# Performance work log

Measured on AMD Instinct MI355X. Metric: run time of the kernel, lower is better.

## Reference

```python
import jax, jax.numpy as jnp
import numpy as np

ALPHA = 0.2          # LeakyReLU negative slope
NEG = -9e15          # masking value from the torch source


def _gat_multihead(x, adj, W, a):
    """All nheads GATLayers (concat=True math, elu applied by caller).
    x: [B,N,F], adj: [B,N,N], W: [H,F,O], a: [H,2O]. Returns [B,H,N,O].
    Note a_input @ a decomposes as h_i.a[:O] + h_j.a[O:], so we never
    materialize the O(N^2 * 2O) pairwise concat tensor."""
    h = jnp.einsum('bnf,hfo->bhno', x, W)            # [B,H,N,O]
    O = h.shape[-1]
    s1 = jnp.einsum('bhno,ho->bhn', h, a[:, :O])     # h_i . a_src
    s2 = jnp.einsum('bhno,ho->bhn', h, a[:, O:])     # h_j . a_dst
    e = jax.nn.leaky_relu(s1[..., :, None] + s2[..., None, :], ALPHA)  # [B,H,N,N]
    att = jax.nn.softmax(jnp.where(adj[:, None] > 0, e, NEG), axis=-1)
    return jnp.einsum('bhij,bhjo->bhio', att, h)


def _gat_single(x, adj, W, a):
    """out_att GATLayer (concat=False, no elu). W: [F,O], a: [2O]."""
    h = jnp.einsum('bnf,fo->bno', x, W)
    O = W.shape[-1]
    s1 = h @ a[:O]
    s2 = h @ a[O:]
    e = jax.nn.leaky_relu(s1[:, :, None] + s2[:, None, :], ALPHA)
    att = jax.nn.softmax(jnp.where(adj > 0, e, NEG), axis=-1)
    return jnp.einsum('bij,bjo->bio', att, h)


def setup_inputs() -> dict:
    key = jax.random.key(0)
    ks = jax.random.split(key, 10)
    B, N, F = 2, 2048, 768
    H, O = 8, 256
    x = jax.random.normal(ks[0], (B, N, F), dtype=jnp.float32)
    # sparse-ish binary adjacency (adj>0 is all that matters) + self loops
    adj = (jax.random.uniform(ks[1], (B, N, N)) < 0.05).astype(jnp.float32)
    adj = jnp.maximum(adj, jnp.eye(N, dtype=jnp.float32)[None])
    mask = jnp.ones((B, N, 1), dtype=jnp.float32)  # unused by GAT.forward
    s = 0.05
    W_heads = jax.random.normal(ks[2], (H, F, O), dtype=jnp.float32) * s
    a_heads = jax.random.normal(ks[3], (H, 2 * O), dtype=jnp.float32) * s
    W_out = jax.random.normal(ks[4], (H * O, O), dtype=jnp.float32) * s
    a_out = jax.random.normal(ks[5], (2 * O,), dtype=jnp.float32) * s
    W_lin = jax.random.normal(ks[6], (O, H * O), dtype=jnp.float32) * s  # nn.Linear weight [out,in]
    b_lin = jnp.zeros((O,), dtype=jnp.float32)
    W_ln = jax.random.normal(ks[7], (O, O), dtype=jnp.float32) * s
    b_ln = jnp.zeros((O,), dtype=jnp.float32)
    return {"x": x, "adj": adj, "mask": mask, "W_heads": W_heads,
            "a_heads": a_heads, "W_out": W_out, "a_out": a_out,
            "W_lin": W_lin, "b_lin": b_lin, "W_ln": W_ln, "b_ln": b_ln}


def reference(x, adj, mask, W_heads, a_heads, W_out, a_out, W_lin, b_lin, W_ln, b_ln):
    # layer 0: multi-head GAT, elu, concat over heads (dropout=0 in eval)
    hp = jax.nn.elu(_gat_multihead(x, adj, W_heads, a_heads))  # [B,H,N,O]
    B, H, N, O = hp.shape
    x1 = jnp.transpose(hp, (0, 2, 1, 3)).reshape(B, N, H * O)
    # layer 1: residual linear + out_att (concat=False)
    x2 = x1 @ W_lin.T + b_lin + _gat_single(x1, adj, W_out, a_out)
    # final: relu(ln(x))
    return jax.nn.relu(x2 @ W_ln.T + b_ln)
```

## Files before the change

### kernel.cpp

```cpp
#include <hip/hip_runtime.h>
#include <hip/hip_bf16.h>

constexpr int Bb = 2, Nn = 2048, Ff = 768, Hh = 8, Oo = 256;

typedef __attribute__((ext_vector_type(8)))  short   short8;
typedef __attribute__((ext_vector_type(16))) float   f32x16;
typedef __attribute__((ext_vector_type(4)))  unsigned short ushort4_t;

__device__ inline unsigned short f2bf(float f) {
    unsigned u = __float_as_uint(f);
    u = (u + 0x7FFFu + ((u >> 16) & 1u)) >> 16;
    return (unsigned short)u;
}

__global__ __launch_bounds__(256) void adjbits_kernel(
        const float* __restrict__ adj, unsigned long long* __restrict__ bits) {
    size_t gid = (size_t)blockIdx.x * 256 + threadIdx.x;
    float v = adj[gid];
    unsigned long long m = __ballot(v > 0.f);
    if ((threadIdx.x & 63) == 0) bits[gid >> 6] = m;
}

__global__ __launch_bounds__(256) void cast_bf_kernel(
        const float* __restrict__ in, unsigned short* __restrict__ out) {
    size_t i = (size_t)blockIdx.x * 256 + threadIdx.x;
    float4 v = ((const float4*)in)[i];
    ushort4_t o;
    o.x = f2bf(v.x); o.y = f2bf(v.y); o.z = f2bf(v.z); o.w = f2bf(v.w);
    ((ushort4_t*)out)[i] = o;
}

__global__ __launch_bounds__(256) void wfrag_kn_kernel(
        const float* __restrict__ W, unsigned short* __restrict__ out,
        int K, int N, long long sW, long long sO) {
    W   += (size_t)blockIdx.y * sW;
    out += (size_t)blockIdx.y * sO;
    int t = threadIdx.x;
    int f = blockIdx.x * 4 + (t >> 6);
    int slot = t & 63, kh = slot >> 5, lm = slot & 31;
    int nfk = K >> 4;
    int nt = f / nfk, kt = f - nt * nfk;
    const float* wp = W + (size_t)(kt * 16 + kh * 8) * N + nt * 32 + lm;
    ushort4_t o0, o1;
    o0.x = f2bf(wp[0]);             o0.y = f2bf(wp[(size_t)N]);
    o0.z = f2bf(wp[2 * (size_t)N]); o0.w = f2bf(wp[3 * (size_t)N]);
    o1.x = f2bf(wp[4 * (size_t)N]); o1.y = f2bf(wp[5 * (size_t)N]);
    o1.z = f2bf(wp[6 * (size_t)N]); o1.w = f2bf(wp[7 * (size_t)N]);
    unsigned short* op = out + (size_t)f * 512 + slot * 8;
    *(ushort4_t*)op = o0;
    *(ushort4_t*)(op + 4) = o1;
}

__global__ __launch_bounds__(256) void wfrag_nk_kernel(
        const float* __restrict__ W, unsigned short* __restrict__ out, int K) {
    int t = threadIdx.x;
    int f = blockIdx.x * 4 + (t >> 6);
    int slot = t & 63, kh = slot >> 5, lm = slot & 31;
    int nfk = K >> 4;
    int nt = f / nfk, kt = f - nt * nfk;
    const float* wp = W + (size_t)(nt * 32 + lm) * K + kt * 16 + kh * 8;
    float4 a = *(const float4*)wp, b = *(const float4*)(wp + 4);
    ushort4_t o0, o1;
    o0.x = f2bf(a.x); o0.y = f2bf(a.y); o0.z = f2bf(a.z); o0.w = f2bf(a.w);
    o1.x = f2bf(b.x); o1.y = f2bf(b.y); o1.z = f2bf(b.z); o1.w = f2bf(b.w);
    unsigned short* op = out + (size_t)f * 512 + slot * 8;
    *(ushort4_t*)op = o0;
    *(ushort4_t*)(op + 4) = o1;
}

__global__ __launch_bounds__(256) void gemm_bf_kernel(
        const unsigned short* __restrict__ A, int K, long long sA, int bAshift,
        const unsigned short* __restrict__ BF, long long sB, int bmask,
        float* __restrict__ C, long long sC,
        unsigned short* __restrict__ CF, long long sCF, int Mtot,
        const float* __restrict__ bias, int mode,
        const float* __restrict__ aall, int amask,
        float* __restrict__ E1p, float* __restrict__ E1n, float2* __restrict__ E2pn) {
    int z = blockIdx.z;
    A  += (size_t)(z >> bAshift) * sA;
    BF += (size_t)(z & bmask) * sB;
    if (C) C += (size_t)z * sC;
    if (CF) CF += (size_t)z * sCF;
    int m0 = blockIdx.x * 64;
    int t = threadIdx.x;
    int wv = t >> 6, lane = t & 63;
    int lm = lane & 31, kh = lane >> 5;
    int nfk = K >> 4;
    __shared__ __align__(16) unsigned short As[64][72];
    f32x16 acc[2][2] = {};
    int sr = t >> 2, sc2 = (t & 3) * 16;
    const unsigned short* ag  = A + (size_t)(m0 + sr) * K + sc2;
    const unsigned short* bg0 = BF + (size_t)(wv * 2) * nfk * 512;
    const unsigned short* bg1 = bg0 + (size_t)nfk * 512;
    for (int k0 = 0; k0 < K; k0 += 64) {
        *(short8*)&As[sr][sc2]     = *(const short8*)(ag + k0);
        *(short8*)&As[sr][sc2 + 8] = *(const short8*)(ag + k0 + 8);
        int kt0 = k0 >> 4;
        __syncthreads();
#pragma unroll
        for (int s = 0; s < 4; ++s) {
            short8 a0 = *(const short8*)&As[lm][s * 16 + kh * 8];
            short8 a1 = *(const short8*)&As[32 + lm][s * 16 + kh * 8];
            short8 b0 = *(const short8*)(bg0 + (size_t)(kt0 + s) * 512 + lane * 8);
            short8 b1 = *(const short8*)(bg1 + (size_t)(kt0 + s) * 512 + lane * 8);
            acc[0][0] = __builtin_amdgcn_mfma_f32_32x32x16_bf16(a0, b0, acc[0][0], 0, 0, 0);
            acc[0][1] = __builtin_amdgcn_mfma_f32_32x32x16_bf16(a0, b1, acc[0][1], 0, 0, 0);
            acc[1][0] = __builtin_amdgcn_mfma_f32_32x32x16_bf16(a1, b0, acc[1][0], 0, 0, 0);
            acc[1][1] = __builtin_amdgcn_mfma_f32_32x32x16_bf16(a1, b1, acc[1][1], 0, 0, 0);
        }
        __syncthreads();
    }
#pragma unroll
    for (int mt = 0; mt < 2; ++mt)
#pragma unroll
        for (int nt = 0; nt < 2; ++nt) {
            int colg = wv * 64 + nt * 32 + lm;
            float bv = (mode == 2) ? bias[colg] : 0.f;
            if (C) {
#pragma unroll
                for (int reg = 0; reg < 16; ++reg) {
                    int rl = mt * 32 + 4 * kh + (reg & 3) + 8 * (reg >> 2);
                    float v = acc[mt][nt][reg];
                    if (mode == 2) { v += bv; v = fmaxf(v, 0.f); }
                    C[(size_t)(m0 + rl) * 256 + colg] = v;
                }
            }
            if (mode == 1) {
#pragma unroll
                for (int q = 0; q < 4; ++q) {
                    int kt = m0 / 16 + mt * 2 + (q >> 1);
                    size_t fi = ((size_t)(colg >> 5) * (Mtot / 16) + kt) * 512 +
                                ((q & 1) * 32 + (colg & 31)) * 8 + kh * 4;
                    ushort4_t pk;
                    pk.x = f2bf(acc[mt][nt][q * 4 + 0]);
                    pk.y = f2bf(acc[mt][nt][q * 4 + 1]);
                    pk.z = f2bf(acc[mt][nt][q * 4 + 2]);
                    pk.w = f2bf(acc[mt][nt][q * 4 + 3]);
                    *(ushort4_t*)(CF + fi) = pk;
                }
            }
        }
    if (aall) {
        const float* av = aall + (size_t)(z & amask) * 512;
        float a1v0 = av[wv * 64 + lm],       a1v1 = av[wv * 64 + 32 + lm];
        float a2v0 = av[256 + wv * 64 + lm], a2v1 = av[256 + wv * 64 + 32 + lm];
        float* sbuf = (float*)As;
#pragma unroll
        for (int mt = 0; mt < 2; ++mt)
#pragma unroll
            for (int reg = 0; reg < 16; ++reg) {
                int rl = mt * 32 + 4 * kh + (reg & 3) + 8 * (reg >> 2);
                float v1 = acc[mt][0][reg] * a1v0 + acc[mt][1][reg] * a1v1;
                float v2 = acc[mt][0][reg] * a2v0 + acc[mt][1][reg] * a2v1;
#pragma unroll
                for (int m = 1; m <= 16; m <<= 1) {
                    v1 += __shfl_xor(v1, m, 64);
                    v2 += __shfl_xor(v2, m, 64);
                }
                if (lm == 0) { sbuf[rl * 8 + wv] = v1; sbuf[rl * 8 + 4 + wv] = v2; }
            }
        __syncthreads();
        if (t < 64) {
            float s1 = sbuf[t * 8] + sbuf[t * 8 + 1] + sbuf[t * 8 + 2] + sbuf[t * 8 + 3];
            float s2 = sbuf[t * 8 + 4] + sbuf[t * 8 + 5] + sbuf[t * 8 + 6] + sbuf[t * 8 + 7];
            size_t ei = (size_t)z * Nn + m0 + t;
            E1p[ei] = __expf(s1);
            E1n[ei] = __expf(0.2f * s1);
            E2pn[ei] = make_float2(__expf(s2), __expf(0.2f * s2));
        }
    }
}

__global__ __launch_bounds__(256) void gemm_dual_kernel(
        const unsigned short* __restrict__ A, int K, long long sA,
        const unsigned short* __restrict__ BF,
        unsigned short* __restrict__ h2f, float* __restrict__ lin,
        const float* __restrict__ a_out,
        float* __restrict__ E1p, float* __restrict__ E1n, float2* __restrict__ E2pn) {
    int b = blockIdx.z, ng = blockIdx.y;
    A += (size_t)b * sA;
    int nfk = K >> 4;
    BF += (size_t)ng * 8 * nfk * 512;
    int m0 = blockIdx.x * 64;
    int t = threadIdx.x;
    int wv = t >> 6, lane = t & 63;
    int lm = lane & 31, kh = lane >> 5;
    __shared__ __align__(16) unsigned short As[64][72];
    f32x16 acc[2][2] = {};
    int sr = t >> 2, sc2 = (t & 3) * 16;
    const unsigned short* ag  = A + (size_t)(m0 + sr) * K + sc2;
    const unsigned short* bg0 = BF + (size_t)(wv * 2) * nfk * 512;
    const unsigned short* bg1 = bg0 + (size_t)nfk * 512;
    for (int k0 = 0; k0 < K; k0 += 64) {
        *(short8*)&As[sr][sc2]     = *(const short8*)(ag + k0);
        *(short8*)&As[sr][sc2 + 8] = *(const short8*)(ag + k0 + 8);
        int kt0 = k0 >> 4;
        __syncthreads();
#pragma unroll
        for (int s = 0; s < 4; ++s) {
            short8 a0 = *(const short8*)&As[lm][s * 16 + kh * 8];
            short8 a1 = *(const short8*)&As[32 + lm][s * 16 + kh * 8];
            short8 b0 = *(const short8*)(bg0 + (size_t)(kt0 + s) * 512 + lane * 8);
            short8 b1 = *(const short8*)(bg1 + (size_t)(kt0 + s) * 512 + lane * 8);
            acc[0][0] = __builtin_amdgcn_mfma_f32_32x32x16_bf16(a0, b0, acc[0][0], 0, 0, 0);
            acc[0][1] = __builtin_amdgcn_mfma_f32_32x32x16_bf16(a0, b1, acc[0][1], 0, 0, 0);
            acc[1][0] = __builtin_amdgcn_mfma_f32_32x32x16_bf16(a1, b0, acc[1][0], 0, 0, 0);
            acc[1][1] = __builtin_amdgcn_mfma_f32_32x32x16_bf16(a1, b1, acc[1][1], 0, 0, 0);
        }
        __syncthreads();
    }
    if (ng == 1) {
        float* C = lin + (size_t)b * Nn * 256;
#pragma unroll
        for (int mt = 0; mt < 2; ++mt)
#pragma unroll
            for (int nt = 0; nt < 2; ++nt) {
                int colg = wv * 64 + nt * 32 + lm;
#pragma unroll
                for (int reg = 0; reg < 16; ++reg) {
                    int rl = mt * 32 + 4 * kh + (reg & 3) + 8 * (reg >> 2);
                    C[(size_t)(m0 + rl) * 256 + colg] = acc[mt][nt][reg];
                }
            }
    } else {
        unsigned short* CF = h2f + (size_t)b * 524288;
#pragma unroll
        for (int mt = 0; mt < 2; ++mt)
#pragma unroll
            for (int nt = 0; nt < 2; ++nt) {
                int colg = wv * 64 + nt * 32 + lm;
#pragma unroll
                for (int q = 0; q < 4; ++q) {
                    int kt = m0 / 16 + mt * 2 + (q >> 1);
                    size_t fi = ((size_t)(colg >> 5) * 128 + kt) * 512 +
                                ((q & 1) * 32 + (colg & 31)) * 8 + kh * 4;
                    ushort4_t pk;
                    pk.x = f2bf(acc[mt][nt][q * 4 + 0]);
                    pk.y = f2bf(acc[mt][nt][q * 4 + 1]);
                    pk.z = f2bf(acc[mt][nt][q * 4 + 2]);
                    pk.w = f2bf(acc[mt][nt][q * 4 + 3]);
                    *(ushort4_t*)(CF + fi) = pk;
                }
            }
        float a1v0 = a_out[wv * 64 + lm],       a1v1 = a_out[wv * 64 + 32 + lm];
        float a2v0 = a_out[256 + wv * 64 + lm], a2v1 = a_out[256 + wv * 64 + 32 + lm];
        float* sbuf = (float*)As;
#pragma unroll
        for (int mt = 0; mt < 2; ++mt)
#pragma unroll
            for (int reg = 0; reg < 16; ++reg) {
                int rl = mt * 32 + 4 * kh + (reg & 3) + 8 * (reg >> 2);
                float v1 = acc[mt][0][reg] * a1v0 + acc[mt][1][reg] * a1v1;
                float v2 = acc[mt][0][reg] * a2v0 + acc[mt][1][reg] * a2v1;
#pragma unroll
                for (int m = 1; m <= 16; m <<= 1) {
                    v1 += __shfl_xor(v1, m, 64);
                    v2 += __shfl_xor(v2, m, 64);
                }
                if (lm == 0) { sbuf[rl * 8 + wv] = v1; sbuf[rl * 8 + 4 + wv] = v2; }
            }
        __syncthreads();
        if (t < 64) {
            float s1 = sbuf[t * 8] + sbuf[t * 8 + 1] + sbuf[t * 8 + 2] + sbuf[t * 8 + 3];
            float s2 = sbuf[t * 8 + 4] + sbuf[t * 8 + 5] + sbuf[t * 8 + 6] + sbuf[t * 8 + 7];
            size_t ei = (size_t)b * Nn + m0 + t;
            E1p[ei] = __expf(s1);
            E1n[ei] = __expf(0.2f * s1);
            E2pn[ei] = make_float2(__expf(s2), __expf(0.2f * s2));
        }
    }
}

template<int JLEN, int MODE, int SWAPXY>
__global__ __launch_bounds__(256, 2) void attn_v7_kernel(
        const unsigned short* __restrict__ hfrag,
        const unsigned* __restrict__ bits,
        const float* __restrict__ E1p, const float* __restrict__ E1n,
        const float2* __restrict__ E2pn,
        unsigned short* __restrict__ outbf, int ldo,
        float* __restrict__ pacc, float* __restrict__ plsum,
        int hshift) {
    constexpr int W = JLEN / 32, NC = JLEN / 64, ABS = W + 1;
    int it = SWAPXY ? blockIdx.y : blockIdx.x;
    int bh = SWAPXY ? blockIdx.x : blockIdx.y;
    int js = blockIdx.z;
    int b = bh >> hshift, hd = bh & ((1 << hshift) - 1);
    int i0 = it * 64, jbase = js * JLEN;
    int kt0 = js * (JLEN / 16);
    int t = threadIdx.x, lane = t & 63;
    int wv = t >> 6, lm = lane & 31, kh = lane >> 5;
    int ti = lane, jq = wv;

    __shared__ unsigned ab[64 * ABS];
    __shared__ __align__(16) unsigned short ps[3][64][64];
    __shared__ float lred[64][5];
    __shared__ float linv[64];

    const unsigned* bb = bits + ((size_t)b * Nn + i0) * 64 + (jbase >> 5);
    for (int k = t; k < 64 * W; k += 256) {
        int r = k / W, w0 = k - r * W;
        ab[r * ABS + w0] = bb[(size_t)r * 64 + w0];
    }
    __syncthreads();

    float e1p = E1p[(size_t)bh * Nn + i0 + ti];
    float e1n = E1n[(size_t)bh * Nn + i0 + ti];
    const float4* e2base = (const float4*)(E2pn + (size_t)bh * Nn + jbase);

    const unsigned short* bg0 = hfrag + (size_t)bh * 524288 + (size_t)(wv * 2) * 128 * 512;
    const unsigned short* bg1 = bg0 + 128 * 512;

    f32x16 acc[2][2] = {};
    float lp0 = 0.f, lp1 = 0.f;
    short8 B0[8], B1[8];

    auto loadB = [&](int c, short8* B) {
#pragma unroll
        for (int s = 0; s < 4; ++s) {
            int kt = kt0 + c * 4 + s;
            B[2 * s]     = *(const short8*)(bg0 + (size_t)kt * 512 + lane * 8);
            B[2 * s + 1] = *(const short8*)(bg1 + (size_t)kt * 512 + lane * 8);
        }
    };
    auto computeP = [&](int c, int buf) {
        int cj = c * 64;
        unsigned word = ab[ti * ABS + ((cj >> 5) + (jq >> 1))];
        unsigned field = word >> ((jq & 1) * 16);
        const float4* ep = e2base + ((cj + jq * 16) >> 1);
        unsigned pk[8];
#pragma unroll
        for (int u = 0; u < 8; ++u) {
            float4 q = ep[u];
            float p0 = fmaxf(e1p * q.x, e1n * q.y);
            p0 = ((field >> (2 * u)) & 1u) ? p0 : 0.f;
            float p1 = fmaxf(e1p * q.z, e1n * q.w);
            p1 = ((field >> (2 * u + 1)) & 1u) ? p1 : 0.f;
            if (u & 1) lp1 += p0 + p1; else lp0 += p0 + p1;
            __hip_bfloat162 hv = __float22bfloat162_rn(make_float2(p0, p1));
            pk[u] = *(unsigned*)&hv;
        }
        unsigned sw = ti & 7;
        uint4 v0; v0.x = pk[0]; v0.y = pk[1]; v0.z = pk[2]; v0.w = pk[3];
        uint4 v1; v1.x = pk[4]; v1.y = pk[5]; v1.z = pk[6]; v1.w = pk[7];
        *(uint4*)&ps[buf][ti][((2 * jq) ^ sw) * 8]     = v0;
        *(uint4*)&ps[buf][ti][((2 * jq + 1) ^ sw) * 8] = v1;
    };
    auto mfmaStep = [&](int buf, short8* B) {
        unsigned sw = lm & 7;
#pragma unroll
        for (int s = 0; s < 4; ++s) {
            short8 a0 = *(const short8*)&ps[buf][lm][((2 * s + kh) ^ sw) * 8];
            short8 a1 = *(const short8*)&ps[buf][32 + lm][((2 * s + kh) ^ sw) * 8];
            acc[0][0] = __builtin_amdgcn_mfma_f32_32x32x16_bf16(a0, B[2 * s],     acc[0][0], 0, 0, 0);
            acc[0][1] = __builtin_amdgcn_mfma_f32_32x32x16_bf16(a0, B[2 * s + 1], acc[0][1], 0, 0, 0);
            acc[1][0] = __builtin_amdgcn_mfma_f32_32x32x16_bf16(a1, B[2 * s],     acc[1][0], 0, 0, 0);
            acc[1][1] = __builtin_amdgcn_mfma_f32_32x32x16_bf16(a1, B[2 * s + 1], acc[1][1], 0, 0, 0);
        }
    };

    computeP(0, 0);
    computeP(1, 1);
    loadB(0, B0);
    loadB(1, B1);
    __syncthreads();
    for (int c = 0; c < NC; ++c) {
        short8* Bc = (c & 1) ? B1 : B0;
        mfmaStep(c % 3, Bc);
        if (c + 2 < NC) {
            computeP(c + 2, (c + 2) % 3);
            loadB(c + 2, Bc);
        }
        __syncthreads();
    }

    lred[ti][jq] = lp0 + lp1;
    __syncthreads();
    if (MODE == 0) {
        if (t < 64) linv[t] = 1.f / (lred[t][0] + lred[t][1] + lred[t][2] + lred[t][3]);
        __syncthreads();
#pragma unroll
        for (int mt = 0; mt < 2; ++mt)
#pragma unroll
            for (int nt = 0; nt < 2; ++nt) {
                int o = wv * 64 + nt * 32 + lm;
#pragma unroll
                for (int reg = 0; reg < 16; ++reg) {
                    int rl = mt * 32 + 4 * kh + (reg & 3) + 8 * (reg >> 2);
                    float v = acc[mt][nt][reg] * linv[rl];
                    v = v > 0.f ? v : expm1f(v);
                    outbf[((size_t)b * Nn + i0 + rl) * ldo + (size_t)hd * Oo + o] = f2bf(v);
                }
            }
    } else {
        if (t < 64)
            plsum[((size_t)js * Bb + b) * Nn + i0 + t] =
                lred[t][0] + lred[t][1] + lred[t][2] + lred[t][3];
        float* pa = pacc + (((size_t)js * Bb + b) * Nn) * 256;
#pragma unroll
        for (int mt = 0; mt < 2; ++mt)
#pragma unroll
            for (int nt = 0; nt < 2; ++nt) {
                int o = wv * 64 + nt * 32 + lm;
#pragma unroll
                for (int reg = 0; reg < 16; ++reg) {
                    int rl = mt * 32 + 4 * kh + (reg & 3) + 8 * (reg >> 2);
                    pa[(size_t)(i0 + rl) * 256 + o] = acc[mt][nt][reg];
                }
            }
    }
}

__global__ __launch_bounds__(256) void combine8_kernel(
        const float* __restrict__ pacc, const float* __restrict__ plsum,
        const float* __restrict__ lin, const float* __restrict__ bias,
        unsigned short* __restrict__ out) {
    int gid = blockIdx.x * 256 + threadIdx.x;
    int row = gid >> 6;
    int o4 = gid & 63;
    size_t ps4 = (size_t)Bb * Nn * 64;
    const float4* p = (const float4*)pacc + (size_t)row * 64 + o4;
    float4 s = p[0];
#pragma unroll
    for (int k = 1; k < 8; ++k) {
        float4 q = p[k * ps4];
        s.x += q.x; s.y += q.y; s.z += q.z; s.w += q.w;
    }
    int BN = Bb * Nn;
    float lsum = 0.f;
#pragma unroll
    for (int k = 0; k < 8; ++k) lsum += plsum[row + k * BN];
    float li = 1.f / lsum;
    float4 lv = ((const float4*)lin)[(size_t)row * 64 + o4];
    float4 bv = ((const float4*)bias)[o4];
    float4 v;
    v.x = s.x * li + lv.x + bv.x; v.y = s.y * li + lv.y + bv.y;
    v.z = s.z * li + lv.z + bv.z; v.w = s.w * li + lv.w + bv.w;
    __hip_bfloat162 h0 = __float22bfloat162_rn(make_float2(v.x, v.y));
    __hip_bfloat162 h1 = __float22bfloat162_rn(make_float2(v.z, v.w));
    uint2 st; st.x = *(unsigned*)&h0; st.y = *(unsigned*)&h1;
    *(uint2*)(out + (size_t)gid * 4) = st;
}

extern "C" void kernel_launch(void* const* d_in, const int* in_sizes, int n_in,
                              void* d_out, int out_size, void* d_ws, size_t ws_size,
                              hipStream_t stream) {
    const float* x       = (const float*)d_in[0];
    const float* adj     = (const float*)d_in[1];
    const float* W_heads = (const float*)d_in[3];
    const float* a_heads = (const float*)d_in[4];
    const float* W_out   = (const float*)d_in[5];
    const float* a_out   = (const float*)d_in[6];
    const float* W_lin   = (const float*)d_in[7];
    const float* b_lin   = (const float*)d_in[8];
    const float* W_ln    = (const float*)d_in[9];
    const float* b_ln    = (const float*)d_in[10];

    char* w = (char*)d_ws;
    float* pacc     = (float*)(w);
    float* lin      = (float*)(w + 33554432);
    float* E1p_mh   = (float*)(w + 41943040);
    float* E1n_mh   = (float*)(w + 42074112);
    float2* E2pn_mh = (float2*)(w + 42205184);
    float* E1p_sh   = (float*)(w + 42467328);
    float* E1n_sh   = (float*)(w + 42483712);
    float2* E2pn_sh = (float2*)(w + 42500096);
    unsigned long long* bits = (unsigned long long*)(w + 42532864);
    unsigned short* x_bf  = (unsigned short*)(w + 43581440);
    unsigned short* x2_bf = (unsigned short*)(w + 43581440);
    unsigned short* WhF   = (unsigned short*)(w + 49872896);
    unsigned short* WoF   = (unsigned short*)(w + 53018624);
    unsigned short* WlF   = (unsigned short*)(w + 54067200);
    unsigned short* WnF   = (unsigned short*)(w + 55115776);
    unsigned short* hfrag = (unsigned short*)(w + 55246848);
    unsigned short* h2frag= (unsigned short*)(w + 72024064);
    unsigned short* x1_bf = (unsigned short*)(w + 74121216);
    float* plsum = E1p_mh;

    adjbits_kernel<<<(Bb * Nn * Nn) / 256, 256, 0, stream>>>(adj, bits);
    cast_bf_kernel<<<(Bb * Nn * Ff) / 1024, 256, 0, stream>>>(x, x_bf);
    wfrag_kn_kernel<<<dim3(96, Hh), 256, 0, stream>>>(
        W_heads, WhF, Ff, Oo, (long long)Ff * Oo, 384LL * 512);
    wfrag_kn_kernel<<<dim3(256, 1), 256, 0, stream>>>(
        W_out, WoF, Hh * Oo, Oo, 0, 0);
    wfrag_nk_kernel<<<256, 256, 0, stream>>>(W_lin, WlF, Hh * Oo);
    wfrag_nk_kernel<<<32, 256, 0, stream>>>(W_ln, WnF, Oo);

    gemm_bf_kernel<<<dim3(Nn / 64, 1, Bb * Hh), 256, 0, stream>>>(
        x_bf, Ff, (long long)Nn * Ff, 3, WhF, 384LL * 512, 7,
        nullptr, 0, hfrag, 524288, Nn, nullptr, 1,
        a_heads, 7, E1p_mh, E1n_mh, E2pn_mh);
    attn_v7_kernel<2048, 0, 1><<<dim3(Bb * Hh, Nn / 64, 1), 256, 0, stream>>>(
        hfrag, (const unsigned*)bits, E1p_mh, E1n_mh, E2pn_mh,
        x1_bf, Hh * Oo, nullptr, nullptr, 3);
    gemm_dual_kernel<<<dim3(Nn / 64, 2, Bb), 256, 0, stream>>>(
        x1_bf, Hh * Oo, (long long)Nn * Hh * Oo, WoF, h2frag, lin,
        a_out, E1p_sh, E1n_sh, E2pn_sh);
    attn_v7_kernel<256, 1, 0><<<dim3(Nn / 64, Bb, 8), 256, 0, stream>>>(
        h2frag, (const unsigned*)bits, E1p_sh, E1n_sh, E2pn_sh,
        nullptr, 0, pacc, plsum, 0);
    combine8_kernel<<<(Bb * Nn * 64) / 256, 256, 0, stream>>>(pacc, plsum, lin, b_lin, x2_bf);
    gemm_bf_kernel<<<dim3(Nn / 64, 1, Bb), 256, 0, stream>>>(
        x2_bf, Oo, (long long)Nn * Oo, 0, WnF, 0, 0,
        (float*)d_out, (long long)Nn * Oo, nullptr, 0, Nn, b_ln, 2,
        nullptr, 0, nullptr, nullptr, nullptr);
}
```

Measured before the change: 295.8 us.

## Halve attention row tile to 32 and pipeline B loads per k-step

The attention kernel now processes 32 query rows per block instead of 64. This doubles the grid, raises the occupancy target from 2 to 4 blocks per CU, and cuts the accumulator and B-register footprint. B fragments are loaded one k-step ahead into a two-slot ping-pong, interleaved with the MFMAs, and the P buffer goes from three to two stages. The aim is better latency hiding and more waves per CU. The cost is that each h fragment is reused across half as many rows, so B-matrix global/L2 traffic doubles.

```diff
diff --git a/kernel.cpp b/kernel.cpp
--- a/kernel.cpp
+++ b/kernel.cpp
@@ -272,7 +272,7 @@
 }
 
 template<int JLEN, int MODE, int SWAPXY>
-__global__ __launch_bounds__(256, 2) void attn_v7_kernel(
+__global__ __launch_bounds__(256, 4) void attn_v8_kernel(
         const unsigned short* __restrict__ hfrag,
         const unsigned* __restrict__ bits,
         const float* __restrict__ E1p, const float* __restrict__ E1n,
@@ -285,19 +285,19 @@
     int bh = SWAPXY ? blockIdx.x : blockIdx.y;
     int js = blockIdx.z;
     int b = bh >> hshift, hd = bh & ((1 << hshift) - 1);
-    int i0 = it * 64, jbase = js * JLEN;
+    int i0 = it * 32, jbase = js * JLEN;
     int kt0 = js * (JLEN / 16);
     int t = threadIdx.x, lane = t & 63;
     int wv = t >> 6, lm = lane & 31, kh = lane >> 5;
-    int ti = lane, jq = wv;
-
-    __shared__ unsigned ab[64 * ABS];
-    __shared__ __align__(16) unsigned short ps[3][64][64];
-    __shared__ float lred[64][5];
-    __shared__ float linv[64];
+    int ti = t & 31, jq = t >> 5;
+
+    __shared__ unsigned ab[32 * ABS];
+    __shared__ __align__(16) unsigned short ps[2][32][64];
+    __shared__ float lred[32][9];
+    __shared__ float linv[32];
 
     const unsigned* bb = bits + ((size_t)b * Nn + i0) * 64 + (jbase >> 5);
-    for (int k = t; k < 64 * W; k += 256) {
+    for (int k = t; k < 32 * W; k += 256) {
         int r = k / W, w0 = k - r * W;
         ab[r * ABS + w0] = bb[(size_t)r * 64 + w0];
     }
@@ -310,26 +310,23 @@
     const unsigned short* bg0 = hfrag + (size_t)bh * 524288 + (size_t)(wv * 2) * 128 * 512;
     const unsigned short* bg1 = bg0 + 128 * 512;
 
-    f32x16 acc[2][2] = {};
+    f32x16 acc[2] = {};
     float lp0 = 0.f, lp1 = 0.f;
-    short8 B0[8], B1[8];
-
-    auto loadB = [&](int c, short8* B) {
-#pragma unroll
-        for (int s = 0; s < 4; ++s) {
-            int kt = kt0 + c * 4 + s;
-            B[2 * s]     = *(const short8*)(bg0 + (size_t)kt * 512 + lane * 8);
-            B[2 * s + 1] = *(const short8*)(bg1 + (size_t)kt * 512 + lane * 8);
-        }
+    short8 Bpp[2][2];
+
+    auto loadBs = [&](int c, int s, int slot) {
+        int kt = kt0 + c * 4 + s;
+        Bpp[slot][0] = *(const short8*)(bg0 + (size_t)kt * 512 + lane * 8);
+        Bpp[slot][1] = *(const short8*)(bg1 + (size_t)kt * 512 + lane * 8);
     };
     auto computeP = [&](int c, int buf) {
         int cj = c * 64;
-        unsigned word = ab[ti * ABS + ((cj >> 5) + (jq >> 1))];
-        unsigned field = word >> ((jq & 1) * 16);
-        const float4* ep = e2base + ((cj + jq * 16) >> 1);
-        unsigned pk[8];
-#pragma unroll
-        for (int u = 0; u < 8; ++u) {
+        unsigned word = ab[ti * ABS + (cj >> 5) + (jq >> 2)];
+        unsigned field = (word >> ((jq & 3) * 8)) & 0xffu;
+        const float4* ep = e2base + ((cj + jq * 8) >> 1);
+        unsigned pk[4];
+#pragma unroll
+        for (int u = 0; u < 4; ++u) {
             float4 q = ep[u];
             float p0 = fmaxf(e1p * q.x, e1n * q.y);
             p0 = ((field >> (2 * u)) & 1u) ? p0 : 0.f;
@@ -339,74 +336,68 @@
             __hip_bfloat162 hv = __float22bfloat162_rn(make_float2(p0, p1));
             pk[u] = *(unsigned*)&hv;
         }
-        unsigned sw = ti & 7;
-        uint4 v0; v0.x = pk[0]; v0.y = pk[1]; v0.z = pk[2]; v0.w = pk[3];
-        uint4 v1; v1.x = pk[4]; v1.y = pk[5]; v1.z = pk[6]; v1.w = pk[7];
-        *(uint4*)&ps[buf][ti][((2 * jq) ^ sw) * 8]     = v0;
-        *(uint4*)&ps[buf][ti][((2 * jq + 1) ^ sw) * 8] = v1;
+        uint4 v; v.x = pk[0]; v.y = pk[1]; v.z = pk[2]; v.w = pk[3];
+        *(uint4*)&ps[buf][ti][(jq ^ (ti & 7)) * 8] = v;
     };
-    auto mfmaStep = [&](int buf, short8* B) {
-        unsigned sw = lm & 7;
-#pragma unroll
-        for (int s = 0; s < 4; ++s) {
-            short8 a0 = *(const short8*)&ps[buf][lm][((2 * s + kh) ^ sw) * 8];
-            short8 a1 = *(const short8*)&ps[buf][32 + lm][((2 * s + kh) ^ sw) * 8];
-            acc[0][0] = __builtin_amdgcn_mfma_f32_32x32x16_bf16(a0, B[2 * s],     acc[0][0], 0, 0, 0);
-            acc[0][1] = __builtin_amdgcn_mfma_f32_32x32x16_bf16(a0, B[2 * s + 1], acc[0][1], 0, 0, 0);
-            acc[1][0] = __builtin_amdgcn_mfma_f32_32x32x16_bf16(a1, B[2 * s],     acc[1][0], 0, 0, 0);
-            acc[1][1] = __builtin_amdgcn_mfma_f32_32x32x16_bf16(a1, B[2 * s + 1], acc[1][1], 0, 0, 0);
-        }
+    auto mfmaS = [&](int buf, int s, int slot) {
+        int g = 2 * s + kh;
+        short8 a0 = *(const short8*)&ps[buf][lm][(g ^ (lm & 7)) * 8];
+        acc[0] = __builtin_amdgcn_mfma_f32_32x32x16_bf16(a0, Bpp[slot][0], acc[0], 0, 0, 0);
+        acc[1] = __builtin_amdgcn_mfma_f32_32x32x16_bf16(a0, Bpp[slot][1], acc[1], 0, 0, 0);
     };
 
     computeP(0, 0);
-    computeP(1, 1);
-    loadB(0, B0);
-    loadB(1, B1);
+    loadBs(0, 0, 0);
     __syncthreads();
     for (int c = 0; c < NC; ++c) {
-        short8* Bc = (c & 1) ? B1 : B0;
-        mfmaStep(c % 3, Bc);
-        if (c + 2 < NC) {
-            computeP(c + 2, (c + 2) % 3);
-            loadB(c + 2, Bc);
-        }
+        int cb = c & 1, nb = cb ^ 1;
+        if (c + 1 < NC) computeP(c + 1, nb);
+        loadBs(c, 1, 1);            mfmaS(cb, 0, 0);
+        loadBs(c, 2, 0);            mfmaS(cb, 1, 1);
+        loadBs(c, 3, 1);            mfmaS(cb, 2, 0);
+        if (c + 1 < NC) loadBs(c + 1, 0, 0);
+        mfmaS(cb, 3, 1);
         __syncthreads();
     }
 
     lred[ti][jq] = lp0 + lp1;
     __syncthreads();
     if (MODE == 0) {
-        if (t < 64) linv[t] = 1.f / (lred[t][0] + lred[t][1] + lred[t][2] + lred[t][3]);
-        __syncthreads();
-#pragma unroll
-        for (int mt = 0; mt < 2; ++mt)
-#pragma unroll
-            for (int nt = 0; nt < 2; ++nt) {
-                int o = wv * 64 + nt * 32 + lm;
-#pragma unroll
-                for (int reg = 0; reg < 16; ++reg) {
-                    int rl = mt * 32 + 4 * kh + (reg & 3) + 8 * (reg >> 2);
-                    float v = acc[mt][nt][reg] * linv[rl];
-                    v = v > 0.f ? v : expm1f(v);
-                    outbf[((size_t)b * Nn + i0 + rl) * ldo + (size_t)hd * Oo + o] = f2bf(v);
-                }
-            }
+        if (t < 32) {
+            float s = 0.f;
+#pragma unroll
+            for (int k = 0; k < 8; ++k) s += lred[t][k];
+            linv[t] = 1.f / s;
+        }
+        __syncthreads();
+#pragma unroll
+        for (int nt = 0; nt < 2; ++nt) {
+            int o = wv * 64 + nt * 32 + lm;
+#pragma unroll
+            for (int reg = 0; reg < 16; ++reg) {
+                int rl = 4 * kh + (reg & 3) + 8 * (reg >> 2);
+                float v = acc[nt][reg] * linv[rl];
+                v = v > 0.f ? v : expm1f(v);
+                outbf[((size_t)b * Nn + i0 + rl) * ldo + (size_t)hd * Oo + o] = f2bf(v);
+            }
+        }
     } else {
-        if (t < 64)
-            plsum[((size_t)js * Bb + b) * Nn + i0 + t] =
-                lred[t][0] + lred[t][1] + lred[t][2] + lred[t][3];
+        if (t < 32) {
+            float s = 0.f;
+#pragma unroll
+            for (int k = 0; k < 8; ++k) s += lred[t][k];
+            plsum[((size_t)js * Bb + b) * Nn + i0 + t] = s;
+        }
         float* pa = pacc + (((size_t)js * Bb + b) * Nn) * 256;
 #pragma unroll
-        for (int mt = 0; mt < 2; ++mt)
-#pragma unroll
-            for (int nt = 0; nt < 2; ++nt) {
-                int o = wv * 64 + nt * 32 + lm;
-#pragma unroll
-                for (int reg = 0; reg < 16; ++reg) {
-                    int rl = mt * 32 + 4 * kh + (reg & 3) + 8 * (reg >> 2);
-                    pa[(size_t)(i0 + rl) * 256 + o] = acc[mt][nt][reg];
-                }
-            }
+        for (int nt = 0; nt < 2; ++nt) {
+            int o = wv * 64 + nt * 32 + lm;
+#pragma unroll
+            for (int reg = 0; reg < 16; ++reg) {
+                int rl = 4 * kh + (reg & 3) + 8 * (reg >> 2);
+                pa[(size_t)(i0 + rl) * 256 + o] = acc[nt][reg];
+            }
+        }
     }
 }
 
@@ -489,13 +480,13 @@
         x_bf, Ff, (long long)Nn * Ff, 3, WhF, 384LL * 512, 7,
         nullptr, 0, hfrag, 524288, Nn, nullptr, 1,
         a_heads, 7, E1p_mh, E1n_mh, E2pn_mh);
-    attn_v7_kernel<2048, 0, 1><<<dim3(Bb * Hh, Nn / 64, 1), 256, 0, stream>>>(
+    attn_v8_kernel<2048, 0, 1><<<dim3(Bb * Hh, Nn / 32, 1), 256, 0, stream>>>(
         hfrag, (const unsigned*)bits, E1p_mh, E1n_mh, E2pn_mh,
         x1_bf, Hh * Oo, nullptr, nullptr, 3);
     gemm_dual_kernel<<<dim3(Nn / 64, 2, Bb), 256, 0, stream>>>(
         x1_bf, Hh * Oo, (long long)Nn * Hh * Oo, WoF, h2frag, lin,
         a_out, E1p_sh, E1n_sh, E2pn_sh);
-    attn_v7_kernel<256, 1, 0><<<dim3(Nn / 64, Bb, 8), 256, 0, stream>>>(
+    attn_v8_kernel<256, 1, 0><<<dim3(Nn / 32, Bb, 8), 256, 0, stream>>>(
         h2frag, (const unsigned*)bits, E1p_sh, E1n_sh, E2pn_sh,
         nullptr, 0, pacc, plsum, 0);
     combine8_kernel<<<(Bb * Nn * 64) / 256, 256, 0, stream>>>(pacc, plsum, lin, b_lin, x2_bf);
```

Measured after the change: 285.6 us. 3.5% less time.
